# Kernel tuning notes

Measured on AMD Instinct MI355X. Metric: run time of the kernel, lower is better.

## Reference

```python
import jax, jax.numpy as jnp
import numpy as np

B, S, D_IN, D_OUT = 4, 2048, 4096, 16384
Q_MAX = 127  # 8-bit symmetric

def setup_inputs() -> dict:
    key = jax.random.key(0)
    k1, k2, k3, k4 = jax.random.split(key, 4)
    x = jax.random.normal(k1, (B, S, D_IN), dtype=jnp.float32)
    # integer weights in [-q_max, q_max], stored as int32 (stand-in for int8)
    weight_int = jax.random.randint(k2, (D_OUT, D_IN), -Q_MAX, Q_MAX + 1, dtype=jnp.int32)
    # per-output-channel positive scales (typical magnitude ~ max|w|/127)
    scale = jax.random.uniform(k3, (D_OUT, 1), dtype=jnp.float32, minval=1e-4, maxval=2e-2)
    bias = jax.random.normal(k4, (D_OUT,), dtype=jnp.float32)
    return {"x": x, "weight_int": weight_int, "scale": scale, "bias": bias}

def reference(x, weight_int, scale, bias):
    # Dequantize weight to activation dtype, then dense matmul (F.linear)
    w = weight_int.astype(x.dtype) * scale.astype(x.dtype)  # (out, in)
    # out[b,s,o] = sum_i x[b,s,i] * w[o,i] + bias[o]
    return jnp.einsum('bsi,oi->bso', x, w) + bias.astype(x.dtype)
```

## Files before the change

kernel.cpp:

```cpp
#include <hip/hip_runtime.h>


typedef __bf16 bf16x8 __attribute__((ext_vector_type(8)));
typedef float floatx4 __attribute__((ext_vector_type(4)));
typedef unsigned short ushort_t;

#define GEMM_M 8192
#define GEMM_N 16384
#define GEMM_K 4096

__device__ inline unsigned int f2bf(float f) {
    unsigned int u = __float_as_uint(f);
    unsigned int r = u + 0x7FFFu + ((u >> 16) & 1u);
    return r >> 16;
}

__global__ __launch_bounds__(256) void cvt_f32_bf16(const float4* __restrict__ in,
                                                    uint4* __restrict__ outp) {
    int i = blockIdx.x * 256 + threadIdx.x;
    float4 a = in[2 * i];
    float4 b = in[2 * i + 1];
    uint4 o;
    o.x = f2bf(a.x) | (f2bf(a.y) << 16);
    o.y = f2bf(a.z) | (f2bf(a.w) << 16);
    o.z = f2bf(b.x) | (f2bf(b.y) << 16);
    o.w = f2bf(b.z) | (f2bf(b.w) << 16);
    outp[i] = o;
}

__global__ __launch_bounds__(256) void cvt_i32_bf16(const int4* __restrict__ in,
                                                    uint4* __restrict__ outp) {
    int i = blockIdx.x * 256 + threadIdx.x;
    int4 a = in[2 * i];
    int4 b = in[2 * i + 1];
    uint4 o;
    o.x = f2bf((float)a.x) | (f2bf((float)a.y) << 16);
    o.y = f2bf((float)a.z) | (f2bf((float)a.w) << 16);
    o.z = f2bf((float)b.x) | (f2bf((float)b.y) << 16);
    o.w = f2bf((float)b.z) | (f2bf((float)b.w) << 16);
    outp[i] = o;
}

#define GLOAD_LDS16(gsrc, ldst)                                                        \
    __builtin_amdgcn_global_load_lds(                                                  \
        (const __attribute__((address_space(1))) void*)(gsrc),                         \
        (__attribute__((address_space(3))) void*)(ldst), 16, 0, 0)

__global__ __launch_bounds__(256) void gemm_bf16(const ushort_t* __restrict__ xb,
                                                 const ushort_t* __restrict__ wb,
                                                 const float* __restrict__ scale,
                                                 const float* __restrict__ bias,
                                                 float* __restrict__ out) {
    __shared__ __align__(16) ushort_t As[128 * 64];
    __shared__ __align__(16) ushort_t Bs[128 * 64];

    const int tid  = threadIdx.x;
    const int wave = tid >> 6;
    const int lane = tid & 63;
    const int q    = lane >> 4;
    const int l16  = lane & 15;
    const int wm   = wave >> 1;
    const int wn   = wave & 1;

    const size_t rowBase = (size_t)blockIdx.y * 128;
    const size_t colBase = (size_t)blockIdx.x * 128;

    const ushort_t* Ag = xb + rowBase * GEMM_K;
    const ushort_t* Bg = wb + colBase * GEMM_K;

    const int srow = tid >> 3;
    const int scol = (((tid & 7) ^ (srow & 7)) << 3);
    const int xr   = l16 & 7;

    floatx4 acc[4][4] = {};

    for (int kt = 0; kt < GEMM_K; kt += 64) {
        __syncthreads();
#pragma unroll
        for (int s = 0; s < 4; ++s) {
            GLOAD_LDS16(Ag + (size_t)(s * 32 + srow) * GEMM_K + kt + scol,
                        &As[(s * 256 + wave * 64) * 8]);
            GLOAD_LDS16(Bg + (size_t)(s * 32 + srow) * GEMM_K + kt + scol,
                        &Bs[(s * 256 + wave * 64) * 8]);
        }
        __syncthreads();

#pragma unroll
        for (int ks = 0; ks < 2; ++ks) {
            bf16x8 af[4], bfr[4];
#pragma unroll
            for (int i = 0; i < 4; ++i) {
                const int m  = wm * 64 + i * 16 + l16;
                const int gA = (ks * 4 + q) ^ xr;
                af[i] = *(const bf16x8*)&As[(m * 8 + gA) * 8];
            }
#pragma unroll
            for (int j = 0; j < 4; ++j) {
                const int n  = wn * 64 + j * 16 + l16;
                const int gB = (ks * 4 + q) ^ xr;
                bfr[j] = *(const bf16x8*)&Bs[(n * 8 + gB) * 8];
            }
#pragma unroll
            for (int i = 0; i < 4; ++i)
#pragma unroll
                for (int j = 0; j < 4; ++j)
                    acc[i][j] = __builtin_amdgcn_mfma_f32_16x16x32_bf16(
                        af[i], bfr[j], acc[i][j], 0, 0, 0);
        }
    }

    float scl[4], bs[4];
#pragma unroll
    for (int j = 0; j < 4; ++j) {
        const size_t col = colBase + wn * 64 + j * 16 + l16;
        scl[j] = scale[col];
        bs[j]  = bias[col];
    }
#pragma unroll
    for (int i = 0; i < 4; ++i) {
        const size_t row0 = rowBase + wm * 64 + i * 16 + q * 4;
#pragma unroll
        for (int r = 0; r < 4; ++r) {
            float* orow = out + (row0 + r) * (size_t)GEMM_N;
#pragma unroll
            for (int j = 0; j < 4; ++j) {
                const size_t col = colBase + wn * 64 + j * 16 + l16;
                orow[col] = acc[i][j][r] * scl[j] + bs[j];
            }
        }
    }
}

extern "C" void kernel_launch(void* const* d_in, const int* in_sizes, int n_in,
                              void* d_out, int out_size, void* d_ws, size_t ws_size,
                              hipStream_t stream) {
    const float* x     = (const float*)d_in[0];
    const int*   w     = (const int*)d_in[1];
    const float* scale = (const float*)d_in[2];
    const float* bias  = (const float*)d_in[3];
    float*       out   = (float*)d_out;

    ushort_t* xb = (ushort_t*)d_ws;
    ushort_t* wb = (ushort_t*)d_ws + (size_t)GEMM_M * GEMM_K;

    cvt_f32_bf16<<<(GEMM_M * (size_t)GEMM_K) / 8 / 256, 256, 0, stream>>>(
        (const float4*)x, (uint4*)xb);
    cvt_i32_bf16<<<((size_t)GEMM_N * GEMM_K) / 8 / 256, 256, 0, stream>>>(
        (const int4*)w, (uint4*)wb);

    dim3 grid(GEMM_N / 128, GEMM_M / 128);
    gemm_bf16<<<grid, dim3(256), 0, stream>>>(xb, wb, scale, bias, out);
}
```

Before: 2.185 ms.

## Rewrite GEMM as 256x256-tile, 8-wave kernel with 4-stage async LDS pipeline

Raises the GEMM tile from 128x128 to 256x256 with 512 threads and a 128 KB LDS ring of four BK=32 stages. Global-to-LDS loads are issued several tiles ahead, with explicit vmcnt waits, barriers and raised MFMA priority so loads overlap with matrix work. It also adds an XCD-aware block swizzle and a new LDS XOR swizzle. The aim is to hide global load latency and raise reuse per block, at the cost of heavy LDS use and hand-written waitcnt scheduling that can be fragile.

Measured after the change: 1.753 ms. -19.8%, faster.

```diff
diff --git a/kernel.cpp b/kernel.cpp
--- a/kernel.cpp
+++ b/kernel.cpp
@@ -8,6 +8,8 @@
 #define GEMM_M 8192
 #define GEMM_N 16384
 #define GEMM_K 4096
+#define BK 32
+#define NTILES (GEMM_K / BK)
 
 __device__ inline unsigned int f2bf(float f) {
     unsigned int u = __float_as_uint(f);
@@ -46,68 +48,122 @@
         (const __attribute__((address_space(1))) void*)(gsrc),                         \
         (__attribute__((address_space(3))) void*)(ldst), 16, 0, 0)
 
-__global__ __launch_bounds__(256) void gemm_bf16(const ushort_t* __restrict__ xb,
-                                                 const ushort_t* __restrict__ wb,
-                                                 const float* __restrict__ scale,
-                                                 const float* __restrict__ bias,
-                                                 float* __restrict__ out) {
-    __shared__ __align__(16) ushort_t As[128 * 64];
-    __shared__ __align__(16) ushort_t Bs[128 * 64];
+#define STAGE_A(tt)                                                                    \
+    do {                                                                               \
+        const int bo_s = ((tt) & 3) * 16384;                                           \
+        GLOAD_LDS16(srcA + (size_t)(tt) * BK, &lds[bo_s + dstA]);                      \
+        GLOAD_LDS16(srcA + (size_t)(tt) * BK + (size_t)16 * GEMM_K,                    \
+                    &lds[bo_s + dstA + 512]);                                          \
+    } while (0)
+
+#define STAGE_B(tt)                                                                    \
+    do {                                                                               \
+        const int bo_s = ((tt) & 3) * 16384;                                           \
+        GLOAD_LDS16(srcB + (size_t)(tt) * BK, &lds[bo_s + dstB]);                      \
+        GLOAD_LDS16(srcB + (size_t)(tt) * BK + (size_t)16 * GEMM_K,                    \
+                    &lds[bo_s + dstB + 512]);                                          \
+    } while (0)
+
+#define VM8 asm volatile("s_waitcnt vmcnt(8)" ::: "memory")
+#define VM4 asm volatile("s_waitcnt vmcnt(4)" ::: "memory")
+#define VM0 asm volatile("s_waitcnt vmcnt(0)" ::: "memory")
+#define VMNONE ((void)0)
+
+#define MFMA16(ACCBASE)                                                                \
+    _Pragma("unroll") for (int i_ = 0; i_ < 4; ++i_)                                   \
+        _Pragma("unroll") for (int j_ = 0; j_ < 4; ++j_)                               \
+            acc[(ACCBASE) + i_][j_] = __builtin_amdgcn_mfma_f32_16x16x32_bf16(         \
+                af[i_], bfr[j_], acc[(ACCBASE) + i_][j_], 0, 0, 0);
+
+#define KTILE(BO, SA, SB, VMW)                                                         \
+    {                                                                                  \
+        bf16x8 af[4], bfr[4];                                                          \
+        _Pragma("unroll") for (int i_ = 0; i_ < 4; ++i_)                               \
+            af[i_] = *(const bf16x8*)&lds[(BO) + aoff + i_ * 512];                     \
+        _Pragma("unroll") for (int j_ = 0; j_ < 4; ++j_)                               \
+            bfr[j_] = *(const bf16x8*)&lds[(BO) + boff + j_ * 512];                    \
+        SA;                                                                            \
+        __builtin_amdgcn_sched_barrier(0);                                             \
+        __builtin_amdgcn_s_barrier();                                                  \
+        asm volatile("s_waitcnt lgkmcnt(0)" ::: "memory");                             \
+        __builtin_amdgcn_sched_barrier(0);                                             \
+        __builtin_amdgcn_s_setprio(1);                                                 \
+        MFMA16(0)                                                                      \
+        __builtin_amdgcn_s_setprio(0);                                                 \
+        __builtin_amdgcn_sched_barrier(0);                                             \
+        __builtin_amdgcn_s_barrier();                                                  \
+        __builtin_amdgcn_sched_barrier(0);                                             \
+        _Pragma("unroll") for (int i_ = 0; i_ < 4; ++i_)                               \
+            af[i_] = *(const bf16x8*)&lds[(BO) + aoff + 2048 + i_ * 512];              \
+        SB;                                                                            \
+        VMW;                                                                           \
+        __builtin_amdgcn_sched_barrier(0);                                             \
+        __builtin_amdgcn_s_barrier();                                                  \
+        asm volatile("s_waitcnt lgkmcnt(0)" ::: "memory");                             \
+        __builtin_amdgcn_sched_barrier(0);                                             \
+        __builtin_amdgcn_s_setprio(1);                                                 \
+        MFMA16(4)                                                                      \
+        __builtin_amdgcn_s_setprio(0);                                                 \
+        __builtin_amdgcn_sched_barrier(0);                                             \
+        __builtin_amdgcn_s_barrier();                                                  \
+        __builtin_amdgcn_sched_barrier(0);                                             \
+    }
+
+__global__ __launch_bounds__(512, 2) void gemm_bf16(const ushort_t* __restrict__ xb,
+                                                    const ushort_t* __restrict__ wb,
+                                                    const float* __restrict__ scale,
+                                                    const float* __restrict__ bias,
+                                                    float* __restrict__ out) {
+    __shared__ __align__(16) ushort_t lds[65536];
 
     const int tid  = threadIdx.x;
     const int wave = tid >> 6;
     const int lane = tid & 63;
+    const int l16  = lane & 15;
     const int q    = lane >> 4;
-    const int l16  = lane & 15;
-    const int wm   = wave >> 1;
-    const int wn   = wave & 1;
-
-    const size_t rowBase = (size_t)blockIdx.y * 128;
-    const size_t colBase = (size_t)blockIdx.x * 128;
-
-    const ushort_t* Ag = xb + rowBase * GEMM_K;
-    const ushort_t* Bg = wb + colBase * GEMM_K;
-
-    const int srow = tid >> 3;
-    const int scol = (((tid & 7) ^ (srow & 7)) << 3);
-    const int xr   = l16 & 7;
-
-    floatx4 acc[4][4] = {};
-
-    for (int kt = 0; kt < GEMM_K; kt += 64) {
-        __syncthreads();
-#pragma unroll
-        for (int s = 0; s < 4; ++s) {
-            GLOAD_LDS16(Ag + (size_t)(s * 32 + srow) * GEMM_K + kt + scol,
-                        &As[(s * 256 + wave * 64) * 8]);
-            GLOAD_LDS16(Bg + (size_t)(s * 32 + srow) * GEMM_K + kt + scol,
-                        &Bs[(s * 256 + wave * 64) * 8]);
-        }
-        __syncthreads();
-
-#pragma unroll
-        for (int ks = 0; ks < 2; ++ks) {
-            bf16x8 af[4], bfr[4];
-#pragma unroll
-            for (int i = 0; i < 4; ++i) {
-                const int m  = wm * 64 + i * 16 + l16;
-                const int gA = (ks * 4 + q) ^ xr;
-                af[i] = *(const bf16x8*)&As[(m * 8 + gA) * 8];
-            }
-#pragma unroll
-            for (int j = 0; j < 4; ++j) {
-                const int n  = wn * 64 + j * 16 + l16;
-                const int gB = (ks * 4 + q) ^ xr;
-                bfr[j] = *(const bf16x8*)&Bs[(n * 8 + gB) * 8];
-            }
-#pragma unroll
-            for (int i = 0; i < 4; ++i)
-#pragma unroll
-                for (int j = 0; j < 4; ++j)
-                    acc[i][j] = __builtin_amdgcn_mfma_f32_16x16x32_bf16(
-                        af[i], bfr[j], acc[i][j], 0, 0, 0);
-        }
-    }
+    const int wm   = wave >> 2;
+    const int wn   = wave & 3;
+
+    const int lin = blockIdx.y * gridDim.x + blockIdx.x;
+    const int swz = (lin & 7) * (2048 / 8) + (lin >> 3);
+    const int bx  = swz & 63;
+    const int by  = swz >> 6;
+    const size_t rowBase = (size_t)by * 256;
+    const size_t colBase = (size_t)bx * 256;
+
+    const int srow = lane >> 2;
+    const int qp   = (lane & 3) ^ ((lane >> 3) & 3);
+    const ushort_t* srcA = xb + (rowBase + (size_t)(wave * 32 + srow)) * GEMM_K + qp * 8;
+    const ushort_t* srcB = wb + (colBase + (size_t)(wave * 32 + srow)) * GEMM_K + qp * 8;
+    const int dstA = wave * 1024;
+    const int dstB = 8192 + wave * 1024;
+
+    const int swzrd = (q ^ ((l16 >> 1) & 3)) << 3;
+    const int aoff  = (wm * 128 + l16) * 32 + swzrd;
+    const int boff  = 8192 + (wn * 64 + l16) * 32 + swzrd;
+
+    floatx4 acc[8][4] = {};
+
+    STAGE_A(0); STAGE_B(0);
+    STAGE_A(1); STAGE_B(1);
+    STAGE_A(2); STAGE_B(2);
+    VM8;
+    __builtin_amdgcn_sched_barrier(0);
+    __builtin_amdgcn_s_barrier();
+    __builtin_amdgcn_sched_barrier(0);
+
+#pragma unroll 1
+    for (int o = 0; o < 31; ++o) {
+        const int t = o * 4;
+        KTILE(0,     STAGE_A(t + 3), STAGE_B(t + 3), VM8);
+        KTILE(16384, STAGE_A(t + 4), STAGE_B(t + 4), VM8);
+        KTILE(32768, STAGE_A(t + 5), STAGE_B(t + 5), VM8);
+        KTILE(49152, STAGE_A(t + 6), STAGE_B(t + 6), VM8);
+    }
+    KTILE(0,     STAGE_A(127), STAGE_B(127), VM8);
+    KTILE(16384, VMNONE, VMNONE, VM4);
+    KTILE(32768, VMNONE, VMNONE, VM0);
+    KTILE(49152, VMNONE, VMNONE, VMNONE);
 
     float scl[4], bs[4];
 #pragma unroll
@@ -117,8 +173,8 @@
         bs[j]  = bias[col];
     }
 #pragma unroll
-    for (int i = 0; i < 4; ++i) {
-        const size_t row0 = rowBase + wm * 64 + i * 16 + q * 4;
+    for (int i = 0; i < 8; ++i) {
+        const size_t row0 = rowBase + wm * 128 + i * 16 + q * 4;
 #pragma unroll
         for (int r = 0; r < 4; ++r) {
             float* orow = out + (row0 + r) * (size_t)GEMM_N;
@@ -148,6 +204,6 @@
     cvt_i32_bf16<<<((size_t)GEMM_N * GEMM_K) / 8 / 256, 256, 0, stream>>>(
         (const int4*)w, (uint4*)wb);
 
-    dim3 grid(GEMM_N / 128, GEMM_M / 128);
-    gemm_bf16<<<grid, dim3(256), 0, stream>>>(xb, wb, scale, bias, out);
-}
+    dim3 grid(GEMM_N / 256, GEMM_M / 256);
+    gemm_bf16<<<grid, dim3(512), 0, stream>>>(xb, wb, scale, bias, out);
+}
```
